# Optimization experiments

Measured on AMD Instinct MI355X. Metric: run time of the kernel, lower is better.

The kernel has to match this reference:

```python
import jax, jax.numpy as jnp
from jax import lax
import numpy as np

HIDDEN = 256

def _lstm_layer(x_tbf, w_ih, w_hh, b_ih, b_hh):
    # x_tbf: [T, B, F]; w_ih: [4H, F]; w_hh: [4H, H]
    B = x_tbf.shape[1]
    # precompute input projections for all timesteps: [T, B, 4H]
    xg = jnp.einsum('tbf,gf->tbg', x_tbf, w_ih) + b_ih + b_hh
    def step(carry, xg_t):
        h, c = carry
        g = xg_t + h @ w_hh.T  # [B, 4H]
        i, f, gg, o = jnp.split(g, 4, axis=-1)  # torch gate order: i, f, g, o
        i = jax.nn.sigmoid(i)
        f = jax.nn.sigmoid(f)
        gg = jnp.tanh(gg)
        o = jax.nn.sigmoid(o)
        c = f * c + i * gg
        h = o * jnp.tanh(c)
        return (h, c), h
    init = (jnp.zeros((B, HIDDEN), x_tbf.dtype), jnp.zeros((B, HIDDEN), x_tbf.dtype))
    _, hs = lax.scan(step, init, xg)
    return hs  # [T, B, H]


def setup_inputs() -> dict:
    key = jax.random.key(0)
    ks = jax.random.split(key, 16)
    B, T, F_IN, NSPK = 64, 1024, 40, 1251
    s = 1.0 / np.sqrt(HIDDEN)
    def u(k, shape):
        return jax.random.uniform(k, shape, jnp.float32, -s, s)
    inp = {'x': jax.random.normal(ks[0], (B, T, F_IN), jnp.float32)}
    in_dims = [F_IN, HIDDEN, HIDDEN]
    ki = 1
    for l in range(3):
        inp[f'w_ih{l}'] = u(ks[ki], (4 * HIDDEN, in_dims[l])); ki += 1
        inp[f'w_hh{l}'] = u(ks[ki], (4 * HIDDEN, HIDDEN)); ki += 1
        inp[f'b_ih{l}'] = u(ks[ki], (4 * HIDDEN,)); ki += 1
        inp[f'b_hh{l}'] = u(ks[ki], (4 * HIDDEN,)); ki += 1
    inp['w_lin'] = u(ks[13], (NSPK, HIDDEN))
    inp['b_lin'] = u(ks[14], (NSPK,))
    return inp


def reference(x, w_ih0, w_hh0, b_ih0, b_hh0, w_ih1, w_hh1, b_ih1, b_hh1,
              w_ih2, w_hh2, b_ih2, b_hh2, w_lin, b_lin):
    # x: [B, T, F] (batch_first). Run 3 stacked LSTM layers.
    h = jnp.transpose(x, (1, 0, 2))  # [T, B, F]
    params = [(w_ih0, w_hh0, b_ih0, b_hh0),
              (w_ih1, w_hh1, b_ih1, b_hh1),
              (w_ih2, w_hh2, b_ih2, b_hh2)]
    for w_ih, w_hh, b_ih, b_hh in params:
        h = _lstm_layer(h, w_ih, w_hh, b_ih, b_hh)
    lstm_out = jnp.transpose(h, (1, 0, 2))  # [B, T, H]
    # Faithful to original: lstm_out[-1] selects the LAST BATCH element -> [T, H]
    last = lstm_out[-1]
    logits = last @ w_lin.T + b_lin  # [T, NSPK]
    return jax.nn.log_softmax(logits, axis=1)
```

## Files before the change

### kernel.cpp

```cpp
#include <hip/hip_runtime.h>

#define HID 256
#define T_STEPS 1024
#define F_IN 40
#define NSPK 1251
#define NCHUNK 8
#define NBLOCKS (3 * NCHUNK)
#define K2_THREADS 512

#define HBUF_WORDS (3 * 1025 * 256)
#define H2F_OFF_BYTES ((size_t)HBUF_WORDS * 8)

__device__ __forceinline__ float fast_sig(float v) {
    return __builtin_amdgcn_rcpf(1.f + __expf(-v));
}
__device__ __forceinline__ float fast_tanh(float v) {
    return 2.f * __builtin_amdgcn_rcpf(1.f + __expf(-2.f * v)) - 1.f;
}

__global__ void k0_init(unsigned long long* __restrict__ hbuf) {
    int tid = threadIdx.x;
    if (tid < 3 * HID) {
        int l = tid / HID, k = tid % HID;
        hbuf[(size_t)(l * 1025 + 0) * HID + k] = 0ull;
    }
}

__global__ __launch_bounds__(K2_THREADS) void k2_lstm(
    const float* __restrict__ x,
    const float* __restrict__ w_ih0, const float* __restrict__ w_hh0,
    const float* __restrict__ b_ih0, const float* __restrict__ b_hh0,
    const float* __restrict__ w_ih1, const float* __restrict__ w_hh1,
    const float* __restrict__ b_ih1, const float* __restrict__ b_hh1,
    const float* __restrict__ w_ih2, const float* __restrict__ w_hh2,
    const float* __restrict__ b_ih2, const float* __restrict__ b_hh2,
    unsigned long long* __restrict__ hbuf, float* __restrict__ h2f)
{
    const int bid = blockIdx.x;
    const int layer = bid / NCHUNK;
    const int g     = bid % NCHUNK;
    const int tid   = threadIdx.x;
    const int seg = tid & 15;
    const int j   = tid >> 4;
    const int jg  = g * 32 + j;

    const float* wih = (layer == 0) ? w_ih0 : (layer == 1) ? w_ih1 : w_ih2;
    const float* whh = (layer == 0) ? w_hh0 : (layer == 1) ? w_hh1 : w_hh2;
    const float* bih = (layer == 0) ? b_ih0 : (layer == 1) ? b_ih1 : b_ih2;
    const float* bhh = (layer == 0) ? b_hh0 : (layer == 1) ? b_hh1 : b_hh2;

    __shared__ float buf[512];
    __shared__ float hv_lds[32];

    float w[4][32];
    float bb[4];
    const int rot = (2 * seg) & 31;
    #pragma unroll
    for (int q = 0; q < 4; q++) {
        const int r = q * 256 + jg;
        bb[q] = bih[r] + bhh[r];
        if (layer > 0) {
            #pragma unroll
            for (int i = 0; i < 32; i++) {
                int k = seg * 32 + ((i + rot) & 31);
                w[q][i] = (k < HID) ? wih[(size_t)r * HID + k]
                                    : whh[(size_t)r * HID + (k - HID)];
            }
        } else {
            #pragma unroll
            for (int i = 0; i < 32; i++) {
                int k = seg * 32 + ((i + rot) & 31);
                w[q][i] = (k < F_IN) ? w_ih0[r * F_IN + k]
                        : (k >= HID) ? whh[(size_t)r * HID + (k - HID)]
                                     : 0.f;
            }
        }
    }

    for (int i = tid; i < 512; i += K2_THREADS) buf[i] = 0.f;
    if (tid < 32) hv_lds[tid] = 0.f;
    __syncthreads();

    const float* x63 = x + 63 * T_STEPS * F_IN;
    const unsigned long long* h_prev_layer = hbuf + (size_t)(layer - 1) * 1025 * HID;
    unsigned long long* h_own              = hbuf + (size_t)layer * 1025 * HID;

    float4 px = make_float4(0.f, 0.f, 0.f, 0.f);
    if (layer == 0 && tid >= 256 && tid < 256 + 10)
        px = ((const float4*)x63)[tid - 256];

    float c_state = 0.f;

    for (int t = 0; t < T_STEPS; t++) {
        if (tid < 256) {
            if ((tid >> 5) == g) {
                buf[256 + tid] = hv_lds[tid & 31];
            } else {
                const unsigned long long* p = h_own + (size_t)t * HID + tid;
                unsigned long long v;
                do {
                    v = __hip_atomic_load(p, __ATOMIC_RELAXED, __HIP_MEMORY_SCOPE_AGENT);
                } while ((unsigned)(v >> 32) != (unsigned)t);
                buf[256 + tid] = __uint_as_float((unsigned)v);
            }
        } else if (layer > 0) {
            const unsigned long long* p = h_prev_layer + (size_t)(t + 1) * HID + (tid - 256);
            unsigned long long v;
            do {
                v = __hip_atomic_load(p, __ATOMIC_RELAXED, __HIP_MEMORY_SCOPE_AGENT);
            } while ((unsigned)(v >> 32) != (unsigned)(t + 1));
            buf[tid - 256] = __uint_as_float((unsigned)v);
        } else if (tid < 256 + 10) {
            ((float4*)buf)[tid - 256] = px;
            if (t + 1 < T_STEPS)
                px = ((const float4*)(x63 + (t + 1) * F_IN))[tid - 256];
        }
        __syncthreads();

        float a0 = 0.f, a1 = 0.f, a2 = 0.f, a3 = 0.f;
        const float* bufs = buf + seg * 32;
        #pragma unroll
        for (int i = 0; i < 32; i++) {
            float f = bufs[(i + rot) & 31];
            a0 += w[0][i] * f;
            a1 += w[1][i] * f;
            a2 += w[2][i] * f;
            a3 += w[3][i] * f;
        }
        #pragma unroll
        for (int m = 1; m < 16; m <<= 1) {
            a0 += __shfl_xor(a0, m, 64);
            a1 += __shfl_xor(a1, m, 64);
            a2 += __shfl_xor(a2, m, 64);
            a3 += __shfl_xor(a3, m, 64);
        }

        if (seg == 0) {
            float si = fast_sig(a0 + bb[0]);
            float sf = fast_sig(a1 + bb[1]);
            float gg = fast_tanh(a2 + bb[2]);
            float so = fast_sig(a3 + bb[3]);
            c_state = sf * c_state + si * gg;
            float hv = so * fast_tanh(c_state);
            hv_lds[j] = hv;
        }
        __syncthreads();

        if (tid < 32) {
            float hv = hv_lds[tid];
            unsigned long long word =
                ((unsigned long long)(unsigned)(t + 1) << 32) | (unsigned long long)__float_as_uint(hv);
            __hip_atomic_store(h_own + (size_t)(t + 1) * HID + g * 32 + tid, word,
                               __ATOMIC_RELAXED, __HIP_MEMORY_SCOPE_AGENT);
            if (layer == 2) h2f[(size_t)t * HID + g * 32 + tid] = hv;
        }
    }
}

#define BM 64
#define BN 64
#define BK 32
__global__ __launch_bounds__(256) void k3_logits(
    const float* __restrict__ A, const float* __restrict__ w_lin,
    const float* __restrict__ b_lin, float* __restrict__ out)
{
    int m0 = blockIdx.x * BM;
    int n0 = blockIdx.y * BN;
    int tid = threadIdx.x;
    __shared__ float As[BM][BK + 1];
    __shared__ float Bs[BN][BK + 1];
    float accv[4][4] = {};
    int tx = tid % 16, ty = tid / 16;

    for (int k0 = 0; k0 < HID; k0 += BK) {
        int row = tid / 4;
        int kq  = (tid % 4) * 8;
        {
            const float4* src = (const float4*)(A + (m0 + row) * HID + k0 + kq);
            float4 v0 = src[0], v1 = src[1];
            As[row][kq + 0] = v0.x; As[row][kq + 1] = v0.y; As[row][kq + 2] = v0.z; As[row][kq + 3] = v0.w;
            As[row][kq + 4] = v1.x; As[row][kq + 5] = v1.y; As[row][kq + 6] = v1.z; As[row][kq + 7] = v1.w;
        }
        {
            int n = n0 + row;
            float4 v0 = make_float4(0.f, 0.f, 0.f, 0.f), v1 = v0;
            if (n < NSPK) {
                const float4* src = (const float4*)(w_lin + n * HID + k0 + kq);
                v0 = src[0]; v1 = src[1];
            }
            Bs[row][kq + 0] = v0.x; Bs[row][kq + 1] = v0.y; Bs[row][kq + 2] = v0.z; Bs[row][kq + 3] = v0.w;
            Bs[row][kq + 4] = v1.x; Bs[row][kq + 5] = v1.y; Bs[row][kq + 6] = v1.z; Bs[row][kq + 7] = v1.w;
        }
        __syncthreads();
        #pragma unroll
        for (int kk = 0; kk < BK; kk++) {
            float a0 = As[ty * 4 + 0][kk], a1 = As[ty * 4 + 1][kk];
            float a2 = As[ty * 4 + 2][kk], a3 = As[ty * 4 + 3][kk];
            float b0 = Bs[tx * 4 + 0][kk], b1 = Bs[tx * 4 + 1][kk];
            float b2 = Bs[tx * 4 + 2][kk], b3 = Bs[tx * 4 + 3][kk];
            accv[0][0] += a0 * b0; accv[0][1] += a0 * b1; accv[0][2] += a0 * b2; accv[0][3] += a0 * b3;
            accv[1][0] += a1 * b0; accv[1][1] += a1 * b1; accv[1][2] += a1 * b2; accv[1][3] += a1 * b3;
            accv[2][0] += a2 * b0; accv[2][1] += a2 * b1; accv[2][2] += a2 * b2; accv[2][3] += a2 * b3;
            accv[3][0] += a3 * b0; accv[3][1] += a3 * b1; accv[3][2] += a3 * b2; accv[3][3] += a3 * b3;
        }
        __syncthreads();
    }
    #pragma unroll
    for (int i = 0; i < 4; i++) {
        int m = m0 + ty * 4 + i;
        #pragma unroll
        for (int j = 0; j < 4; j++) {
            int n = n0 + tx * 4 + j;
            if (n < NSPK) out[(size_t)m * NSPK + n] = accv[i][j] + b_lin[n];
        }
    }
}

__global__ __launch_bounds__(256) void k4_logsoftmax(float* __restrict__ out)
{
    int t = blockIdx.x;
    float* row = out + (size_t)t * NSPK;
    int tid = threadIdx.x;
    __shared__ float red[8];
    float vals[5];
    float lmax = -1e30f;
    #pragma unroll
    for (int k = 0; k < 5; k++) {
        int n = tid + k * 256;
        vals[k] = (n < NSPK) ? row[n] : -1e30f;
        lmax = fmaxf(lmax, vals[k]);
    }
    #pragma unroll
    for (int m = 1; m < 64; m <<= 1) lmax = fmaxf(lmax, __shfl_xor(lmax, m, 64));
    int wave = tid >> 6;
    if ((tid & 63) == 0) red[wave] = lmax;
    __syncthreads();
    float gmax = fmaxf(fmaxf(red[0], red[1]), fmaxf(red[2], red[3]));
    float lsum = 0.f;
    #pragma unroll
    for (int k = 0; k < 5; k++) {
        int n = tid + k * 256;
        if (n < NSPK) lsum += __expf(vals[k] - gmax);
    }
    #pragma unroll
    for (int m = 1; m < 64; m <<= 1) lsum += __shfl_xor(lsum, m, 64);
    if ((tid & 63) == 0) red[4 + wave] = lsum;
    __syncthreads();
    float lse = logf(red[4] + red[5] + red[6] + red[7]) + gmax;
    #pragma unroll
    for (int k = 0; k < 5; k++) {
        int n = tid + k * 256;
        if (n < NSPK) row[n] = vals[k] - lse;
    }
}

extern "C" void kernel_launch(void* const* d_in, const int* in_sizes, int n_in,
                              void* d_out, int out_size, void* d_ws, size_t ws_size,
                              hipStream_t stream) {
    const float* x     = (const float*)d_in[0];
    const float* w_ih0 = (const float*)d_in[1];
    const float* w_hh0 = (const float*)d_in[2];
    const float* b_ih0 = (const float*)d_in[3];
    const float* b_hh0 = (const float*)d_in[4];
    const float* w_ih1 = (const float*)d_in[5];
    const float* w_hh1 = (const float*)d_in[6];
    const float* b_ih1 = (const float*)d_in[7];
    const float* b_hh1 = (const float*)d_in[8];
    const float* w_ih2 = (const float*)d_in[9];
    const float* w_hh2 = (const float*)d_in[10];
    const float* b_ih2 = (const float*)d_in[11];
    const float* b_hh2 = (const float*)d_in[12];
    const float* w_lin = (const float*)d_in[13];
    const float* b_lin = (const float*)d_in[14];

    unsigned long long* hbuf = (unsigned long long*)d_ws;
    float* h2f = (float*)((char*)d_ws + H2F_OFF_BYTES);
    float* out = (float*)d_out;

    k0_init<<<1, 1024, 0, stream>>>(hbuf);
    k2_lstm<<<NBLOCKS, K2_THREADS, 0, stream>>>(
        x, w_ih0, w_hh0, b_ih0, b_hh0,
        w_ih1, w_hh1, b_ih1, b_hh1,
        w_ih2, w_hh2, b_ih2, b_hh2,
        hbuf, h2f);
    k3_logits<<<dim3(16, 20), 256, 0, stream>>>(h2f, w_lin, b_lin, out);
    k4_logsoftmax<<<T_STEPS, 256, 0, stream>>>(out);
}
```

Before: 1.972 ms.

## Spread layer blocks across XCDs and pipeline polling loads for step flags

```diff
diff --git a/kernel.cpp b/kernel.cpp
--- a/kernel.cpp
+++ b/kernel.cpp
@@ -5,7 +5,7 @@
 #define F_IN 40
 #define NSPK 1251
 #define NCHUNK 8
-#define NBLOCKS (3 * NCHUNK)
+#define NBLOCKS 64
 #define K2_THREADS 512
 
 #define HBUF_WORDS (3 * 1025 * 256)
@@ -16,6 +16,19 @@
 }
 __device__ __forceinline__ float fast_tanh(float v) {
     return 2.f * __builtin_amdgcn_rcpf(1.f + __expf(-2.f * v)) - 1.f;
+}
+
+__device__ __forceinline__ float poll_word(const unsigned long long* p, unsigned want) {
+    unsigned long long v0 = __hip_atomic_load(p, __ATOMIC_RELAXED, __HIP_MEMORY_SCOPE_AGENT);
+    if ((unsigned)(v0 >> 32) == want) return __uint_as_float((unsigned)v0);
+    unsigned long long v1 = __hip_atomic_load(p, __ATOMIC_RELAXED, __HIP_MEMORY_SCOPE_AGENT);
+    unsigned long long v2 = __hip_atomic_load(p, __ATOMIC_RELAXED, __HIP_MEMORY_SCOPE_AGENT);
+    unsigned long long v3 = __hip_atomic_load(p, __ATOMIC_RELAXED, __HIP_MEMORY_SCOPE_AGENT);
+    for (;;) {
+        if ((unsigned)(v0 >> 32) == want) return __uint_as_float((unsigned)v0);
+        v0 = v1; v1 = v2; v2 = v3;
+        v3 = __hip_atomic_load(p, __ATOMIC_RELAXED, __HIP_MEMORY_SCOPE_AGENT);
+    }
 }
 
 __global__ void k0_init(unsigned long long* __restrict__ hbuf) {
@@ -37,8 +50,10 @@
     unsigned long long* __restrict__ hbuf, float* __restrict__ h2f)
 {
     const int bid = blockIdx.x;
-    const int layer = bid / NCHUNK;
-    const int g     = bid % NCHUNK;
+    const int xslot = bid & 7;
+    if (xslot >= 3) return;
+    const int layer = xslot;
+    const int g     = bid >> 3;
     const int tid   = threadIdx.x;
     const int seg = tid & 15;
     const int j   = tid >> 4;
@@ -96,20 +111,11 @@
             if ((tid >> 5) == g) {
                 buf[256 + tid] = hv_lds[tid & 31];
             } else {
-                const unsigned long long* p = h_own + (size_t)t * HID + tid;
-                unsigned long long v;
-                do {
-                    v = __hip_atomic_load(p, __ATOMIC_RELAXED, __HIP_MEMORY_SCOPE_AGENT);
-                } while ((unsigned)(v >> 32) != (unsigned)t);
-                buf[256 + tid] = __uint_as_float((unsigned)v);
+                buf[256 + tid] = poll_word(h_own + (size_t)t * HID + tid, (unsigned)t);
             }
         } else if (layer > 0) {
-            const unsigned long long* p = h_prev_layer + (size_t)(t + 1) * HID + (tid - 256);
-            unsigned long long v;
-            do {
-                v = __hip_atomic_load(p, __ATOMIC_RELAXED, __HIP_MEMORY_SCOPE_AGENT);
-            } while ((unsigned)(v >> 32) != (unsigned)(t + 1));
-            buf[tid - 256] = __uint_as_float((unsigned)v);
+            buf[tid - 256] = poll_word(h_prev_layer + (size_t)(t + 1) * HID + (tid - 256),
+                                       (unsigned)(t + 1));
         } else if (tid < 256 + 10) {
             ((float4*)buf)[tid - 256] = px;
             if (t + 1 < T_STEPS)
```

New measurement: 1.864 ms. 5.5% less time.
